# Kernel optimization log

Hardware: AMD Instinct MI355X
Metric: run time of the kernel (lower is better)

Reference implementation:

```python
import jax, jax.numpy as jnp
import numpy as np
import math

B, S, C, H = 32, 500, 1024, 16
D = C // H  # head dim = 64

def setup_inputs() -> dict:
    key = jax.random.key(0)
    ks = jax.random.split(key, 9)
    sc = 1.0 / math.sqrt(C)
    return {
        "x": jax.random.normal(ks[0], (B, S, C), dtype=jnp.float32),
        "Wq": jax.random.normal(ks[1], (C, C), dtype=jnp.float32) * sc,
        "bq": jnp.zeros((C,), dtype=jnp.float32),
        "Wk": jax.random.normal(ks[2], (C, C), dtype=jnp.float32) * sc,
        "bk": jnp.zeros((C,), dtype=jnp.float32),
        "Wv": jax.random.normal(ks[3], (C, C), dtype=jnp.float32) * sc,
        "bv": jnp.zeros((C,), dtype=jnp.float32),
        "Wp": jax.random.normal(ks[4], (C, C), dtype=jnp.float32) * sc,
        "bp": jnp.zeros((C,), dtype=jnp.float32),
    }

def reference(x, Wq, bq, Wk, bk, Wv, bv, Wp, bp):
    # Projections -> [B, H, S, D]
    q = (x @ Wq + bq).reshape(B, S, H, D).transpose(0, 2, 1, 3)
    k = (x @ Wk + bk).reshape(B, S, H, D).transpose(0, 2, 1, 3)
    v = (x @ Wv + bv).reshape(B, S, H, D).transpose(0, 2, 1, 3)
    # Scaled scores [B, H, S, S]
    att = jnp.einsum('bhqd,bhkd->bhqk', q, k) * (1.0 / math.sqrt(D))
    causal = jnp.tril(jnp.ones((S, S), dtype=bool))
    att = jnp.where(causal[None, None], att, jnp.float32(-1e10))
    att = jax.nn.softmax(att, axis=-1)
    # (dropout is identity in eval mode)
    y = jnp.einsum('bhqk,bhkd->bhqd', att, v)  # [B, H, S, D]
    y = y.transpose(0, 2, 1, 3).reshape(B, S, C)
    return y @ Wp + bp
```

## Files before the change

### kernel.cpp

```cpp
#include <hip/hip_runtime.h>
#include <math.h>

#define B_ 32
#define S_ 500
#define C_ 1024
#define H_ 16
#define D_ 64
#define M_ (B_ * S_)
#define MP 16128
#define SP 512

typedef _Float16 f16;
typedef f16 f16x8 __attribute__((ext_vector_type(8)));
typedef f16 f16x4 __attribute__((ext_vector_type(4)));
typedef float f32x4 __attribute__((ext_vector_type(4)));

#define GLOBAL_AS __attribute__((address_space(1)))
#define LDS_AS __attribute__((address_space(3)))

__device__ __forceinline__ void async_load16(const void* g, void* l) {
    __builtin_amdgcn_global_load_lds((const GLOBAL_AS void*)g, (LDS_AS void*)l, 16, 0, 0);
}
template <int N>
__device__ __forceinline__ void wait_vmcnt() {
    asm volatile("s_waitcnt vmcnt(%0)" ::"i"(N) : "memory");
}

struct MaskF { static constexpr bool value = false; };
struct MaskT { static constexpr bool value = true; };

__global__ __launch_bounds__(256) void cast_rows(
    const float* __restrict__ in, f16* __restrict__ out, int n8_real, int n8_tot)
{
    int i = blockIdx.x * 256 + threadIdx.x;
    if (i >= n8_tot) return;
    f16x8 h;
    if (i < n8_real) {
        float4 a = ((const float4*)in)[2 * i];
        float4 b = ((const float4*)in)[2 * i + 1];
        h[0] = (f16)a.x; h[1] = (f16)a.y; h[2] = (f16)a.z; h[3] = (f16)a.w;
        h[4] = (f16)b.x; h[5] = (f16)b.y; h[6] = (f16)b.z; h[7] = (f16)b.w;
    } else {
        f16 z = (f16)0.f;
        h[0] = z; h[1] = z; h[2] = z; h[3] = z;
        h[4] = z; h[5] = z; h[6] = z; h[7] = z;
    }
    ((f16x8*)out)[i] = h;
}

__global__ __launch_bounds__(256) void castW_T4(
    const float* __restrict__ W0, const float* __restrict__ W1,
    const float* __restrict__ W2, const float* __restrict__ W3,
    f16* __restrict__ T0, f16* __restrict__ T1,
    f16* __restrict__ T2, f16* __restrict__ T3)
{
    __shared__ float t[32][33];
    const int z = blockIdx.z;
    const float* W = (z == 0) ? W0 : (z == 1) ? W1 : (z == 2) ? W2 : W3;
    f16* T = (z == 0) ? T0 : (z == 1) ? T1 : (z == 2) ? T2 : T3;
    const int n0 = blockIdx.x * 32, k0 = blockIdx.y * 32;
    const int tx = threadIdx.x, ty = threadIdx.y;
#pragma unroll
    for (int i = 0; i < 4; ++i)
        t[ty + 8 * i][tx] = W[(size_t)(k0 + ty + 8 * i) * C_ + n0 + tx];
    __syncthreads();
#pragma unroll
    for (int i = 0; i < 4; ++i) {
        int n = ty + 8 * i;
        T[(size_t)(n0 + n) * C_ + k0 + tx] = (f16)t[tx][n];
    }
}

#define BAR()                          \
    __builtin_amdgcn_s_barrier();      \
    __builtin_amdgcn_sched_barrier(0)

#define LD_A(MH)                                                              \
    _Pragma("unroll") for (int i = 0; i < 4; ++i)                             \
    _Pragma("unroll") for (int ks = 0; ks < 2; ++ks)                          \
        af[i][ks] = *(const f16x8*)(smem + c * 32768 + rowA +                 \
                                    ((MH) * 64 + i * 16) * 64 + sw[ks]);

#define LD_B(NH)                                                              \
    _Pragma("unroll") for (int j = 0; j < 2; ++j)                             \
    _Pragma("unroll") for (int ks = 0; ks < 2; ++ks)                          \
        bf[NH][j][ks] = *(const f16x8*)(smem + c * 32768 + rowB +             \
                                        ((NH) * 32 + j * 16) * 64 + sw[ks]);

#define MMA(MH, NH)                                                           \
    __builtin_amdgcn_s_setprio(1);                                            \
    _Pragma("unroll") for (int i = 0; i < 4; ++i)                             \
    _Pragma("unroll") for (int j = 0; j < 2; ++j)                             \
    _Pragma("unroll") for (int ks = 0; ks < 2; ++ks)                          \
        acc[(MH) * 4 + i][(NH) * 2 + j] =                                     \
            __builtin_amdgcn_mfma_f32_16x16x32_f16(                           \
                af[i][ks], bf[NH][j][ks], acc[(MH) * 4 + i][(NH) * 2 + j],    \
                0, 0, 0);                                                     \
    __builtin_amdgcn_s_setprio(0)

template <int MODE>
__global__ __launch_bounds__(512) void gemm256(
    const f16* __restrict__ A, const f16* __restrict__ W,
    const float* __restrict__ b0, const float* __restrict__ b1,
    const float* __restrict__ b2, void* __restrict__ o0,
    void* __restrict__ o1, void* __restrict__ o2)
{
    constexpr int K = C_;
    constexpr int NB = (MODE == 0) ? 12 : 4;
    constexpr int NWG = 63 * NB;
    constexpr int Q8 = NWG / 8, R8 = NWG % 8;
    extern __shared__ __align__(16) f16 smem[];

    const int tid = threadIdx.x;
    const int lane = tid & 63, w = tid >> 6;
    const int wm = w >> 2, wn = w & 3;
    const int quad = lane >> 4, lr = lane & 15;

    const int lin = blockIdx.x;
    const int xcd = lin & 7, pos = lin >> 3;
    const int wg = (xcd < R8 ? xcd * (Q8 + 1) : R8 * (Q8 + 1) + (xcd - R8) * Q8) + pos;
    const int m0 = (wg / NB) * 256;
    const int n0 = (wg % NB) * 256;

    const int srow = tid >> 3, sj = tid & 7;
    const int gc = sj ^ (srow & 7);
    const f16* pA = A + (size_t)(m0 + srow) * K + gc * 8;
    const f16* pB = W + (size_t)(n0 + srow) * K + gc * 8;
    f16* dA = smem + tid * 8;
    f16* dB = smem + 16384 + tid * 8;

    auto stageA = [&](int kt, int cb, int h) __attribute__((always_inline)) {
        const f16* s = pA + (size_t)(h * 128) * K + kt * 64;
        f16* d = dA + cb * 32768 + h * 8192;
        async_load16(s, d);
        async_load16(s + (size_t)64 * K, d + 4096);
    };
    auto stageB = [&](int kt, int cb, int h) __attribute__((always_inline)) {
        const f16* s = pB + (size_t)(h * 128) * K + kt * 64;
        f16* d = dB + cb * 32768 + h * 8192;
        async_load16(s, d);
        async_load16(s + (size_t)64 * K, d + 4096);
    };

    int sw[2];
    sw[0] = ((0 + quad) ^ (lr & 7)) * 8;
    sw[1] = ((4 + quad) ^ (lr & 7)) * 8;
    const int rowA = (wm * 128 + lr) * 64;
    const int rowB = 16384 + (wn * 64 + lr) * 64;

    f32x4 acc[8][4];
#pragma unroll
    for (int i = 0; i < 8; ++i)
#pragma unroll
        for (int j = 0; j < 4; ++j) acc[i][j] = (f32x4)0.f;
    f16x8 af[4][2], bf[2][2][2];

    stageA(0, 0, 0); stageA(0, 0, 1); stageB(0, 0, 0); stageB(0, 0, 1);

    constexpr int NT = K / 64;
    for (int kt = 0; kt < NT; ++kt) {
        const int c = kt & 1;
        BAR();
        if (kt + 1 < NT) {
            stageA(kt + 1, c ^ 1, 0); stageA(kt + 1, c ^ 1, 1);
            stageB(kt + 1, c ^ 1, 0); stageB(kt + 1, c ^ 1, 1);
            wait_vmcnt<8>();
        } else {
            wait_vmcnt<0>();
        }
        BAR();
        LD_A(0); LD_B(0);
        MMA(0, 0);
        LD_B(1);
        MMA(0, 1);
        LD_A(1);
        MMA(1, 1);
        MMA(1, 0);
    }

#pragma unroll
    for (int nf = 0; nf < 4; ++nf) {
        int gcn = n0 + wn * 64 + nf * 16 + lr;
        if (MODE == 1) {
            float bv = b0[gcn];
            float* of = (float*)o0;
#pragma unroll
            for (int mf = 0; mf < 8; ++mf) {
                int gr0 = m0 + wm * 128 + mf * 16 + quad * 4;
                if (gr0 >= M_) continue;
#pragma unroll
                for (int r = 0; r < 4; ++r)
                    of[(size_t)(gr0 + r) * C_ + gcn] = acc[mf][nf][r] + bv;
            }
        } else {
            int sec = gcn >> 10;
            int gcl = gcn & 1023;
            const float* bp = (sec == 0) ? b0 : (sec == 1) ? b1 : b2;
            float bv = bp[gcl];
            float osc = (sec == 0) ? 0.125f : 1.0f;
            int h = gcl >> 6, d = gcl & 63;
#pragma unroll
            for (int mf = 0; mf < 8; ++mf) {
                int gr0 = m0 + wm * 128 + mf * 16 + quad * 4;
                if (gr0 >= M_) continue;
                int b = gr0 / S_, s0 = gr0 - b * S_;
                if (sec < 2) {
                    f16* oq = (f16*)((sec == 0) ? o0 : o1);
#pragma unroll
                    for (int r = 0; r < 4; ++r) {
                        float v = (acc[mf][nf][r] + bv) * osc;
                        size_t idx = (((size_t)b * H_ + h) * S_ + (s0 + r)) * D_ + d;
                        oq[idx] = (f16)v;
                    }
                } else {
                    f16* ov = (f16*)o2;
                    f16x4 pk;
#pragma unroll
                    for (int r = 0; r < 4; ++r) pk[r] = (f16)(acc[mf][nf][r] + bv);
                    *(f16x4*)(ov + (((size_t)b * H_ + h) * D_ + d) * SP + s0) = pk;
                }
            }
        }
    }
}

__global__ __launch_bounds__(256, 4) void attn_mfma(
    const f16* __restrict__ qg, const f16* __restrict__ kg,
    const f16* __restrict__ vt, f16* __restrict__ Y)
{
    __shared__ __align__(16) f16 sP[4 * 32 * 64];

    const int tid = threadIdx.x;
    const int lin = blockIdx.x;
    const int xcd = lin & 7;
    const int pos = lin >> 3;
    const int bh = xcd * 64 + (pos >> 2);
    const int qt = 3 - (pos & 3);
    const int q0 = qt * 128;
    const int lane = tid & 63, w = tid >> 6;
    const int quad = lane >> 4, lr = lane & 15;
    const size_t gbase = (size_t)bh * S_ * D_;
    const size_t vbase = (size_t)bh * D_ * SP;
    const int psw = (lr & 7) << 1;

    f16x8 qf[2][2];
#pragma unroll
    for (int t = 0; t < 2; ++t) {
        int q = q0 + w * 32 + t * 16 + lr;
        const f16* pq = qg + gbase + (size_t)q * D_;
#pragma unroll
        for (int s2 = 0; s2 < 2; ++s2)
            qf[t][s2] = *(const f16x8*)(pq + quad * 8 + 32 * s2);
    }

    f32x4 accO[2][4];
#pragma unroll
    for (int t = 0; t < 2; ++t)
#pragma unroll
        for (int nt = 0; nt < 4; ++nt) accO[t][nt] = (f32x4)0.f;
    float l_run[2] = {0.f, 0.f};

    auto step = [&](int kt, auto masked_tag) __attribute__((always_inline)) {
        constexpr bool MASKED = decltype(masked_tag)::value;
        const int k0 = kt * 64;

        f32x4 accS[4][2];
#pragma unroll
        for (int mt = 0; mt < 4; ++mt)
#pragma unroll
            for (int t = 0; t < 2; ++t) accS[mt][t] = (f32x4)0.f;
        __builtin_amdgcn_s_setprio(1);
#pragma unroll
        for (int mt = 0; mt < 4; ++mt) {
            const f16* pk_ = kg + gbase + (size_t)(k0 + mt * 16 + lr) * D_;
#pragma unroll
            for (int s2 = 0; s2 < 2; ++s2) {
                f16x8 ka = *(const f16x8*)(pk_ + quad * 8 + 32 * s2);
#pragma unroll
                for (int t = 0; t < 2; ++t)
                    accS[mt][t] = __builtin_amdgcn_mfma_f32_16x16x32_f16(
                        ka, qf[t][s2], accS[mt][t], 0, 0, 0);
            }
        }
        __builtin_amdgcn_s_setprio(0);

        float ls[2] = {0.f, 0.f};
#pragma unroll
        for (int mt = 0; mt < 4; ++mt)
#pragma unroll
            for (int t = 0; t < 2; ++t) {
                f16x4 pk;
#pragma unroll
                for (int r = 0; r < 4; ++r) {
                    float s = accS[mt][t][r];
                    if (MASKED) {
                        int key = k0 + mt * 16 + quad * 4 + r;
                        int qq = q0 + w * 32 + t * 16 + lr;
                        s = (key <= qq && key < S_) ? s : -1e30f;
                    }
                    float p = __expf(s);
                    ls[t] += p;
                    pk[r] = (f16)p;
                }
                int c8 = (mt * 4 + quad) ^ psw;
                *(f16x4*)&sP[w * 2048 + (t * 16 + lr) * 64 + c8 * 4] = pk;
            }
        ls[0] += __shfl_xor(ls[0], 16); ls[0] += __shfl_xor(ls[0], 32);
        ls[1] += __shfl_xor(ls[1], 16); ls[1] += __shfl_xor(ls[1], 32);
        l_run[0] += ls[0];
        l_run[1] += ls[1];

        __builtin_amdgcn_s_setprio(1);
#pragma unroll
        for (int t = 0; t < 2; ++t) {
            int pb = w * 2048 + (t * 16 + lr) * 64;
#pragma unroll
            for (int s2 = 0; s2 < 2; ++s2) {
                int c8 = (quad * 2 + 8 * s2) ^ psw;
                f16x8 pf = *(const f16x8*)&sP[pb + c8 * 4];
#pragma unroll
                for (int nt = 0; nt < 4; ++nt) {
                    f16x8 vf = *(const f16x8*)(vt + vbase +
                        (size_t)(nt * 16 + lr) * SP + k0 + quad * 8 + s2 * 32);
                    accO[t][nt] = __builtin_amdgcn_mfma_f32_16x16x32_f16(
                        pf, vf, accO[t][nt], 0, 0, 0);
                }
            }
        }
        __builtin_amdgcn_s_setprio(0);
    };

    for (int kt = 0; kt < 2 * qt; ++kt) step(kt, MaskF{});
    step(2 * qt, MaskT{});
    step(2 * qt + 1, MaskT{});

    const int b = bh >> 4, h = bh & 15;
#pragma unroll
    for (int t = 0; t < 2; ++t) {
#pragma unroll
        for (int r = 0; r < 4; ++r) {
            float lsum = __shfl(l_run[t], quad * 4 + r);
            float iv = 1.f / lsum;
            int s = q0 + w * 32 + t * 16 + quad * 4 + r;
            if (s >= S_) continue;
            size_t rowbase = (size_t)(b * S_ + s) * C_ + h * 64;
#pragma unroll
            for (int nt = 0; nt < 4; ++nt)
                Y[rowbase + nt * 16 + lr] = (f16)(accO[t][nt][r] * iv);
        }
    }
}

extern "C" void kernel_launch(void* const* d_in, const int* in_sizes, int n_in,
                              void* d_out, int out_size, void* d_ws, size_t ws_size,
                              hipStream_t stream)
{
    const float* x = (const float*)d_in[0];
    const float* Wq = (const float*)d_in[1];
    const float* bq = (const float*)d_in[2];
    const float* Wk = (const float*)d_in[3];
    const float* bk = (const float*)d_in[4];
    const float* Wv = (const float*)d_in[5];
    const float* bv = (const float*)d_in[6];
    const float* Wp = (const float*)d_in[7];
    const float* bp = (const float*)d_in[8];

    const size_t NEL = (size_t)M_ * C_;
    const size_t WEL = (size_t)C_ * C_;
    f16* qf = (f16*)d_ws;
    f16* kf = qf + NEL;
    f16* vtw = kf + NEL;
    f16* xf = vtw + (size_t)B_ * H_ * D_ * SP;
    f16* wpf = xf + (size_t)MP * C_;
    f16* yf = xf;

    f16* wq = (f16*)d_out;
    f16* wk = wq + WEL;
    f16* wv = wk + WEL;

    hipFuncSetAttribute(reinterpret_cast<const void*>(&gemm256<0>),
                        hipFuncAttributeMaxDynamicSharedMemorySize, 131072);
    hipFuncSetAttribute(reinterpret_cast<const void*>(&gemm256<1>),
                        hipFuncAttributeMaxDynamicSharedMemorySize, 131072);

    castW_T4<<<dim3(32, 32, 4), dim3(32, 8), 0, stream>>>(
        Wq, Wk, Wv, Wp, wq, wk, wv, wpf);

    int n8r = (int)(NEL / 8);
    int n8t = (int)((size_t)MP * C_ / 8);
    cast_rows<<<(n8t + 255) / 256, 256, 0, stream>>>(x, xf, n8r, n8t);

    gemm256<0><<<756, 512, 131072, stream>>>(xf, wq, bq, bk, bv, qf, kf, vtw);

    attn_mfma<<<2048, 256, 0, stream>>>(qf, kf, vtw, yf);

    gemm256<1><<<252, 512, 131072, stream>>>(yf, wpf, bp, nullptr, nullptr,
                                             d_out, nullptr, nullptr);
}
```

Measured before the change: 437.2 us.

## Stage K/V tiles in LDS for attention and merge cast kernels into one launch

The attention kernel now loads each 64-key K tile and V^T tile cooperatively into swizzled LDS with async global-to-LDS loads, then reads MFMA operands from LDS instead of each wave fetching them directly from global memory. This removes redundant global/L2 reads across the four waves. The weight-transpose cast and the input cast are fused into a single prep launch to save one kernel launch. The cost is two block barriers per key tile, with no double buffering so load latency is exposed, and the launch-bounds occupancy hint of 4 is dropped.

New measurement: 368.6 us. 1.19x faster.

```diff
diff --git a/kernel.cpp b/kernel.cpp
--- a/kernel.cpp
+++ b/kernel.cpp
@@ -29,45 +29,46 @@
 struct MaskF { static constexpr bool value = false; };
 struct MaskT { static constexpr bool value = true; };
 
-__global__ __launch_bounds__(256) void cast_rows(
-    const float* __restrict__ in, f16* __restrict__ out, int n8_real, int n8_tot)
-{
-    int i = blockIdx.x * 256 + threadIdx.x;
-    if (i >= n8_tot) return;
-    f16x8 h;
-    if (i < n8_real) {
-        float4 a = ((const float4*)in)[2 * i];
-        float4 b = ((const float4*)in)[2 * i + 1];
-        h[0] = (f16)a.x; h[1] = (f16)a.y; h[2] = (f16)a.z; h[3] = (f16)a.w;
-        h[4] = (f16)b.x; h[5] = (f16)b.y; h[6] = (f16)b.z; h[7] = (f16)b.w;
-    } else {
-        f16 z = (f16)0.f;
-        h[0] = z; h[1] = z; h[2] = z; h[3] = z;
-        h[4] = z; h[5] = z; h[6] = z; h[7] = z;
-    }
-    ((f16x8*)out)[i] = h;
-}
-
-__global__ __launch_bounds__(256) void castW_T4(
+__global__ __launch_bounds__(256) void prep(
+    const float* __restrict__ x, f16* __restrict__ xf, int n8_real, int n8_tot,
     const float* __restrict__ W0, const float* __restrict__ W1,
     const float* __restrict__ W2, const float* __restrict__ W3,
     f16* __restrict__ T0, f16* __restrict__ T1,
     f16* __restrict__ T2, f16* __restrict__ T3)
 {
     __shared__ float t[32][33];
-    const int z = blockIdx.z;
-    const float* W = (z == 0) ? W0 : (z == 1) ? W1 : (z == 2) ? W2 : W3;
-    f16* T = (z == 0) ? T0 : (z == 1) ? T1 : (z == 2) ? T2 : T3;
-    const int n0 = blockIdx.x * 32, k0 = blockIdx.y * 32;
-    const int tx = threadIdx.x, ty = threadIdx.y;
-#pragma unroll
-    for (int i = 0; i < 4; ++i)
-        t[ty + 8 * i][tx] = W[(size_t)(k0 + ty + 8 * i) * C_ + n0 + tx];
-    __syncthreads();
-#pragma unroll
-    for (int i = 0; i < 4; ++i) {
-        int n = ty + 8 * i;
-        T[(size_t)(n0 + n) * C_ + k0 + tx] = (f16)t[tx][n];
+    const int bid = blockIdx.x;
+    const int tid = threadIdx.x;
+    if (bid < 4096) {
+        const int z = bid >> 10, rem = bid & 1023;
+        const float* W = (z == 0) ? W0 : (z == 1) ? W1 : (z == 2) ? W2 : W3;
+        f16* T = (z == 0) ? T0 : (z == 1) ? T1 : (z == 2) ? T2 : T3;
+        const int n0 = (rem & 31) * 32, k0 = (rem >> 5) * 32;
+        const int tx = tid & 31, ty = tid >> 5;
+#pragma unroll
+        for (int i = 0; i < 4; ++i)
+            t[ty + 8 * i][tx] = W[(size_t)(k0 + ty + 8 * i) * C_ + n0 + tx];
+        __syncthreads();
+#pragma unroll
+        for (int i = 0; i < 4; ++i) {
+            int n = ty + 8 * i;
+            T[(size_t)(n0 + n) * C_ + k0 + tx] = (f16)t[tx][n];
+        }
+    } else {
+        int i = (bid - 4096) * 256 + tid;
+        if (i >= n8_tot) return;
+        f16x8 h;
+        if (i < n8_real) {
+            float4 a = ((const float4*)x)[2 * i];
+            float4 b = ((const float4*)x)[2 * i + 1];
+            h[0] = (f16)a.x; h[1] = (f16)a.y; h[2] = (f16)a.z; h[3] = (f16)a.w;
+            h[4] = (f16)b.x; h[5] = (f16)b.y; h[6] = (f16)b.z; h[7] = (f16)b.w;
+        } else {
+            f16 z8 = (f16)0.f;
+            h[0] = z8; h[1] = z8; h[2] = z8; h[3] = z8;
+            h[4] = z8; h[5] = z8; h[6] = z8; h[7] = z8;
+        }
+        ((f16x8*)xf)[i] = h;
     }
 }
 
@@ -224,10 +225,12 @@
     }
 }
 
-__global__ __launch_bounds__(256, 4) void attn_mfma(
+__global__ __launch_bounds__(256) void attn_mfma(
     const f16* __restrict__ qg, const f16* __restrict__ kg,
     const f16* __restrict__ vt, f16* __restrict__ Y)
 {
+    __shared__ __align__(16) f16 sK[64 * 64];
+    __shared__ __align__(16) f16 sVt[64 * 64];
     __shared__ __align__(16) f16 sP[4 * 32 * 64];
 
     const int tid = threadIdx.x;
@@ -260,9 +263,18 @@
         for (int nt = 0; nt < 4; ++nt) accO[t][nt] = (f32x4)0.f;
     float l_run[2] = {0.f, 0.f};
 
-    auto step = [&](int kt, auto masked_tag) __attribute__((always_inline)) {
+    auto iter = [&](int kt, auto masked_tag) __attribute__((always_inline)) {
         constexpr bool MASKED = decltype(masked_tag)::value;
         const int k0 = kt * 64;
+#pragma unroll
+        for (int it = 0; it < 2; ++it) {
+            int idx = it * 256 + tid;
+            int row = idx >> 3, c = idx & 7;
+            int csw = (c ^ (row & 7)) * 8;
+            async_load16(kg + gbase + (size_t)(k0 + row) * D_ + csw, &sK[idx * 8]);
+            async_load16(vt + vbase + (size_t)row * SP + k0 + csw, &sVt[idx * 8]);
+        }
+        __syncthreads();
 
         f32x4 accS[4][2];
 #pragma unroll
@@ -272,10 +284,11 @@
         __builtin_amdgcn_s_setprio(1);
 #pragma unroll
         for (int mt = 0; mt < 4; ++mt) {
-            const f16* pk_ = kg + gbase + (size_t)(k0 + mt * 16 + lr) * D_;
+            int row = mt * 16 + lr;
 #pragma unroll
             for (int s2 = 0; s2 < 2; ++s2) {
-                f16x8 ka = *(const f16x8*)(pk_ + quad * 8 + 32 * s2);
+                int off = row * 64 + (((quad + 4 * s2) ^ (lr & 7)) << 3);
+                f16x8 ka = *(const f16x8*)&sK[off];
 #pragma unroll
                 for (int t = 0; t < 2; ++t)
                     accS[mt][t] = __builtin_amdgcn_mfma_f32_16x16x32_f16(
@@ -320,19 +333,20 @@
                 f16x8 pf = *(const f16x8*)&sP[pb + c8 * 4];
 #pragma unroll
                 for (int nt = 0; nt < 4; ++nt) {
-                    f16x8 vf = *(const f16x8*)(vt + vbase +
-                        (size_t)(nt * 16 + lr) * SP + k0 + quad * 8 + s2 * 32);
+                    f16x8 vf = *(const f16x8*)
+                        &sVt[(nt * 16 + lr) * 64 + (((quad + 4 * s2) ^ (lr & 7)) << 3)];
                     accO[t][nt] = __builtin_amdgcn_mfma_f32_16x16x32_f16(
                         pf, vf, accO[t][nt], 0, 0, 0);
                 }
             }
         }
         __builtin_amdgcn_s_setprio(0);
+        __syncthreads();
     };
 
-    for (int kt = 0; kt < 2 * qt; ++kt) step(kt, MaskF{});
-    step(2 * qt, MaskT{});
-    step(2 * qt + 1, MaskT{});
+    for (int kt = 0; kt < 2 * qt; ++kt) iter(kt, MaskF{});
+    iter(2 * qt, MaskT{});
+    iter(2 * qt + 1, MaskT{});
 
     const int b = bh >> 4, h = bh & 15;
 #pragma unroll
@@ -383,12 +397,11 @@
     hipFuncSetAttribute(reinterpret_cast<const void*>(&gemm256<1>),
                         hipFuncAttributeMaxDynamicSharedMemorySize, 131072);
 
-    castW_T4<<<dim3(32, 32, 4), dim3(32, 8), 0, stream>>>(
-        Wq, Wk, Wv, Wp, wq, wk, wv, wpf);
-
     int n8r = (int)(NEL / 8);
     int n8t = (int)((size_t)MP * C_ / 8);
-    cast_rows<<<(n8t + 255) / 256, 256, 0, stream>>>(x, xf, n8r, n8t);
+    int nprep = 4096 + (n8t + 255) / 256;
+    prep<<<nprep, 256, 0, stream>>>(x, xf, n8r, n8t,
+                                    Wq, Wk, Wv, Wp, wq, wk, wv, wpf);
 
     gemm256<0><<<756, 512, 131072, stream>>>(xf, wq, bq, bk, bv, qf, kf, vtw);
 
```
